# Kernel tuning notes

Hardware: AMD Instinct MI355X
Metric: run time of the kernel (lower is better)

The kernel has to match this reference:

```python
import jax, jax.numpy as jnp
import numpy as np

OUTPUT_SIZE = 16384          # number of map units (must be a perfect square)
SIDE = 128.0                 # sqrt(OUTPUT_SIZE)
SIGMA = 2.0                  # neighbourhood std-dev (non-trainable weight in original)
B, D = 2048, 256


def setup_inputs() -> dict:
    key = jax.random.key(0)
    k1, k2 = jax.random.split(key)
    x = jax.random.normal(k1, (B, D), dtype=jnp.float32)
    kernel = jax.random.normal(k2, (D, OUTPUT_SIZE), dtype=jnp.float32) * 0.1
    return {"x": x, "kernel": kernel}


def _grid_coords():
    # 2D coordinates of each flattened map unit: unit k -> (k // side, k % side)
    idx = jnp.arange(OUTPUT_SIZE, dtype=jnp.float32)
    return jnp.floor(idx / SIDE), jnp.mod(idx, SIDE)  # each (size,)


def reference(x, kernel):
    # Squared Euclidean distance of every sample to every prototype: (B, size).
    # Same math as tf.norm(x[:, :, None] - kernel[None])**2, expressed as a GEMM.
    norms2 = (jnp.sum(x * x, axis=1, keepdims=True)
              - 2.0 * (x @ kernel)
              + jnp.sum(kernel * kernel, axis=0, keepdims=True))
    norms2 = jnp.maximum(norms2, 0.0)

    # Winner-take-all unit per sample, mapped to 2D grid coordinates.
    wta = jnp.argmin(norms2, axis=1).astype(jnp.float32)        # (B,)
    mean_r = jnp.floor(wta / SIDE)                               # (B,)
    mean_c = jnp.mod(wta, SIDE)                                  # (B,)

    # Gaussian neighbourhood over the 2D grid, flattened: (B, size).
    gr, gc = _grid_coords()
    dr = gr[None, :] - mean_r[:, None]
    dc = gc[None, :] - mean_c[:, None]
    radials = jnp.exp(-0.5 / (SIGMA * SIGMA) * (dr * dr + dc * dc))

    return radials * norms2
```

## Files before the change

### kernel.cpp

```cpp
#include <hip/hip_runtime.h>
#include <hip/hip_fp16.h>

#define OUTN 16384
#define BATCH 2048
#define DIM   256
#define NCB   (OUTN / 128)

typedef _Float16 half8 __attribute__((ext_vector_type(8)));
typedef float    floatx4 __attribute__((ext_vector_type(4)));
typedef unsigned long long u64;

__device__ __forceinline__ void gl2lds16(const void* g, void* l) {
    __builtin_amdgcn_global_load_lds(
        (const __attribute__((address_space(1))) void*)g,
        (__attribute__((address_space(3))) void*)l, 16, 0, 0);
}

__device__ __forceinline__ u64 packkey(float v, int col) {
    unsigned u = __float_as_uint(v);
    u = (u & 0x80000000u) ? ~u : (u | 0x80000000u);
    return ((u64)u << 32) | (unsigned)col;
}
__device__ __forceinline__ float unpackval(u64 p) {
    unsigned u = (unsigned)(p >> 32);
    u = (u & 0x80000000u) ? (u & 0x7fffffffu) : ~u;
    return __uint_as_float(u);
}

__global__ void prep_x(const float* __restrict__ x, _Float16* __restrict__ xh,
                       float* __restrict__ rown) {
    int b = blockIdx.x, t = threadIdx.x;
    float v = x[b * DIM + t];
    xh[b * DIM + t] = (_Float16)v;
    float s = v * v;
    for (int off = 32; off; off >>= 1) s += __shfl_down(s, off, 64);
    __shared__ float wsum[4];
    if ((t & 63) == 0) wsum[t >> 6] = s;
    __syncthreads();
    if (t == 0) rown[b] = wsum[0] + wsum[1] + wsum[2] + wsum[3];
}

__global__ __launch_bounds__(256) void prep_kTn(const float* __restrict__ kern,
                                                _Float16* __restrict__ kT,
                                                float* __restrict__ coln) {
    __shared__ float tile[64][65];
    __shared__ float npart[4][64];
    int t = threadIdx.x, tx = t & 63, ty = t >> 6;
    int j0 = blockIdx.x * 64;
    float nrm = 0.f;
    for (int dc = 0; dc < DIM; dc += 64) {
        __syncthreads();
        for (int it = 0; it < 16; it++) {
            int d = dc + ty + it * 4;
            float v = kern[(size_t)d * OUTN + j0 + tx];
            tile[ty + it * 4][tx] = v;
            nrm = fmaf(v, v, nrm);
        }
        __syncthreads();
        for (int c = t; c < 512; c += 256) {
            int j = c >> 3, o8 = (c & 7) * 8;
            half8 h;
            for (int u = 0; u < 8; u++) h[u] = (_Float16)tile[o8 + u][j];
            *(half8*)&kT[(size_t)(j0 + j) * DIM + dc + o8] = h;
        }
    }
    npart[ty][tx] = nrm;
    __syncthreads();
    if (t < 64) coln[j0 + t] = npart[0][t] + npart[1][t] + npart[2][t] + npart[3][t];
}

__global__ __launch_bounds__(256) void gemm_norms(
        const _Float16* __restrict__ xh, const _Float16* __restrict__ kT,
        const float* __restrict__ rown, const float* __restrict__ coln,
        float* __restrict__ out, u64* __restrict__ blockcand) {
    __shared__ __align__(16) char smem[32768];
    _Float16* As = (_Float16*)smem;
    _Float16* Bs = (_Float16*)(smem + 16384);
    u64* cand = (u64*)smem;
    int tid  = threadIdx.x;
    int col0 = blockIdx.x * 128;
    int row0 = blockIdx.y * 128;
    int wid = tid >> 6, lane = tid & 63;
    int wr = wid >> 1, wc = wid & 1;
    int l15 = lane & 15, l4 = lane >> 4;

    floatx4 acc[4][4];
    for (int i = 0; i < 4; i++)
        for (int j = 0; j < 4; j++)
            acc[i][j] = (floatx4){0.f, 0.f, 0.f, 0.f};

    for (int kt = 0; kt < 4; kt++) {
        int k0 = kt * 64;
        for (int it = 0; it < 4; it++) {
            int chunk = it * 256 + tid;
            int r = chunk >> 3, k8 = (chunk & 7) * 8;
            gl2lds16(&xh[(size_t)(row0 + r) * DIM + k0 + k8], &As[chunk * 8]);
            gl2lds16(&kT[(size_t)(col0 + r) * DIM + k0 + k8], &Bs[chunk * 8]);
        }
        __syncthreads();
        for (int s = 0; s < 2; s++) {
            int kk = s * 32 + l4 * 8;
            half8 af[4], bf[4];
            for (int i = 0; i < 4; i++)
                af[i] = *(half8*)&As[(wr * 64 + i * 16 + l15) * 64 + kk];
            for (int j = 0; j < 4; j++)
                bf[j] = *(half8*)&Bs[(wc * 64 + j * 16 + l15) * 64 + kk];
            for (int i = 0; i < 4; i++)
                for (int j = 0; j < 4; j++)
                    acc[i][j] = __builtin_amdgcn_mfma_f32_16x16x32_f16(
                        af[i], bf[j], acc[i][j], 0, 0, 0);
        }
        __syncthreads();
    }

    float cn[4]; int oc[4];
    for (int j = 0; j < 4; j++) {
        oc[j] = col0 + wc * 64 + j * 16 + l15;
        cn[j] = coln[oc[j]];
    }
    for (int i = 0; i < 4; i++) {
        for (int r = 0; r < 4; r++) {
            int row_l = wr * 64 + i * 16 + l4 * 4 + r;
            int orow  = row0 + row_l;
            float rn = rown[orow];
            u64 best = ~0ull;
            for (int j = 0; j < 4; j++) {
                float val = rn + cn[j] - 2.0f * acc[i][j][r];
                out[(size_t)orow * OUTN + oc[j]] = val;
                u64 p = packkey(val, oc[j]);
                if (p < best) best = p;
            }
            cand[row_l * 32 + wc * 16 + l15] = best;
        }
    }
    __syncthreads();
    if (tid < 128) {
        u64 m1 = ~0ull, m2 = ~0ull;
        for (int s = 0; s < 32; s++) {
            u64 v = cand[tid * 32 + s];
            if (v < m1) { m2 = m1; m1 = v; }
            else if (v < m2) { m2 = v; }
        }
        size_t base = (size_t)(row0 + tid) * (NCB * 2) + blockIdx.x * 2;
        blockcand[base]     = m1;
        blockcand[base + 1] = m2;
    }
}

__global__ __launch_bounds__(256) void refine_finalize(
        const u64* __restrict__ blockcand, const float* __restrict__ x,
        const float* __restrict__ kern, const float* __restrict__ coln,
        float* __restrict__ out) {
    int b = blockIdx.x, t = threadIdx.x;
    __shared__ float xrow[DIM];
    __shared__ u64 red[256];
    xrow[t] = x[b * DIM + t];
    u64 e = blockcand[(size_t)b * 256 + t];
    red[t] = e;
    __syncthreads();
    for (int off = 128; off; off >>= 1) {
        if (t < off) { u64 o = red[t + off]; if (o < red[t]) red[t] = o; }
        __syncthreads();
    }
    float minv = unpackval(red[0]);
    __syncthreads();

    float ve = unpackval(e);
    u64 p = ~0ull;
    if (ve <= minv + 0.125f) {
        int j = (int)(e & 0xffffffffu);
        float dot = 0.f;
        for (int d = 0; d < DIM; d++)
            dot = fmaf(xrow[d], kern[(size_t)d * OUTN + j], dot);
        p = packkey(coln[j] - 2.0f * dot, j);
    }
    red[t] = p;
    __syncthreads();
    for (int off = 128; off; off >>= 1) {
        if (t < off) { u64 o = red[t + off]; if (o < red[t]) red[t] = o; }
        __syncthreads();
    }
    int w = (int)(red[0] & 0xffffffffu);
    int wrr = w >> 7, wcc = w & 127;

    float* rowp = out + (size_t)b * OUTN;
    for (int it = 0; it < 16; it++) {
        int idx4 = it * 256 + t;
        int j0 = idx4 * 4;
        int r  = j0 >> 7, c0 = j0 & 127;
        int dr = r - wrr, drsq = dr * dr;
        float4 res;
        {
            int dc = c0 - wcc;     int d2 = drsq + dc * dc;
            res.x = (d2 <= 720) ? __expf(-0.125f * (float)d2) * fmaxf(rowp[j0], 0.f) : 0.f;
        }
        {
            int dc = c0 + 1 - wcc; int d2 = drsq + dc * dc;
            res.y = (d2 <= 720) ? __expf(-0.125f * (float)d2) * fmaxf(rowp[j0 + 1], 0.f) : 0.f;
        }
        {
            int dc = c0 + 2 - wcc; int d2 = drsq + dc * dc;
            res.z = (d2 <= 720) ? __expf(-0.125f * (float)d2) * fmaxf(rowp[j0 + 2], 0.f) : 0.f;
        }
        {
            int dc = c0 + 3 - wcc; int d2 = drsq + dc * dc;
            res.w = (d2 <= 720) ? __expf(-0.125f * (float)d2) * fmaxf(rowp[j0 + 3], 0.f) : 0.f;
        }
        ((float4*)rowp)[idx4] = res;
    }
}

extern "C" void kernel_launch(void* const* d_in, const int* in_sizes, int n_in,
                              void* d_out, int out_size, void* d_ws, size_t ws_size,
                              hipStream_t stream) {
    const float* x    = (const float*)d_in[0];
    const float* kern = (const float*)d_in[1];
    float* out = (float*)d_out;
    char* ws = (char*)d_ws;

    _Float16* xh   = (_Float16*)(ws);
    _Float16* kT   = (_Float16*)(ws + (1u << 20));
    float*    coln = (float*)(ws + (9u << 20));
    float*    rown = (float*)(ws + (9u << 20) + 65536);
    u64* blockcand = (u64*)(ws + (10u << 20));

    prep_x<<<BATCH, DIM, 0, stream>>>(x, xh, rown);
    prep_kTn<<<OUTN / 64, 256, 0, stream>>>(kern, kT, coln);
    gemm_norms<<<dim3(OUTN / 128, BATCH / 128), 256, 0, stream>>>(xh, kT, rown, coln, out, blockcand);
    refine_finalize<<<BATCH, 256, 0, stream>>>(blockcand, x, kern, coln, out);
}
```

Before: 206.2 us.

## Merge prep kernels, swizzle LDS tiles, and stage distances in fp16 workspace

Combines the x and kernel prep kernels into one launch, splitting the kernel transpose over two D halves so more blocks run, with partial column norms summed later. Adds an XOR swizzle to the LDS layout in the GEMM to avoid bank conflicts on MFMA fragment reads. When the workspace is large enough, the intermediate squared distances are stored as fp16 in the workspace instead of fp32 in the output, and the finalize pass only reads values inside the Gaussian cutoff. This aims to halve intermediate write and read traffic, at the cost of fp16 rounding on the stored distances.

```diff
diff --git a/kernel.cpp b/kernel.cpp
--- a/kernel.cpp
+++ b/kernel.cpp
@@ -4,7 +4,6 @@
 #define OUTN 16384
 #define BATCH 2048
 #define DIM   256
-#define NCB   (OUTN / 128)
 
 typedef _Float16 half8 __attribute__((ext_vector_type(8)));
 typedef float    floatx4 __attribute__((ext_vector_type(4)));
@@ -27,52 +26,58 @@
     return __uint_as_float(u);
 }
 
-__global__ void prep_x(const float* __restrict__ x, _Float16* __restrict__ xh,
-                       float* __restrict__ rown) {
-    int b = blockIdx.x, t = threadIdx.x;
-    float v = x[b * DIM + t];
-    xh[b * DIM + t] = (_Float16)v;
-    float s = v * v;
-    for (int off = 32; off; off >>= 1) s += __shfl_down(s, off, 64);
-    __shared__ float wsum[4];
-    if ((t & 63) == 0) wsum[t >> 6] = s;
-    __syncthreads();
-    if (t == 0) rown[b] = wsum[0] + wsum[1] + wsum[2] + wsum[3];
-}
-
-__global__ __launch_bounds__(256) void prep_kTn(const float* __restrict__ kern,
-                                                _Float16* __restrict__ kT,
-                                                float* __restrict__ coln) {
-    __shared__ float tile[64][65];
-    __shared__ float npart[4][64];
-    int t = threadIdx.x, tx = t & 63, ty = t >> 6;
-    int j0 = blockIdx.x * 64;
-    float nrm = 0.f;
-    for (int dc = 0; dc < DIM; dc += 64) {
-        __syncthreads();
-        for (int it = 0; it < 16; it++) {
-            int d = dc + ty + it * 4;
-            float v = kern[(size_t)d * OUTN + j0 + tx];
-            tile[ty + it * 4][tx] = v;
-            nrm = fmaf(v, v, nrm);
-        }
-        __syncthreads();
-        for (int c = t; c < 512; c += 256) {
-            int j = c >> 3, o8 = (c & 7) * 8;
-            half8 h;
-            for (int u = 0; u < 8; u++) h[u] = (_Float16)tile[o8 + u][j];
-            *(half8*)&kT[(size_t)(j0 + j) * DIM + dc + o8] = h;
-        }
-    }
-    npart[ty][tx] = nrm;
-    __syncthreads();
-    if (t < 64) coln[j0 + t] = npart[0][t] + npart[1][t] + npart[2][t] + npart[3][t];
-}
-
+__global__ __launch_bounds__(256) void prep_all(
+        const float* __restrict__ x, const float* __restrict__ kern,
+        _Float16* __restrict__ xh, float* __restrict__ rown,
+        _Float16* __restrict__ kT, float* __restrict__ colnp) {
+    int blk = blockIdx.x, t = threadIdx.x;
+    if (blk < 512) {
+        __shared__ float tile[64][65];
+        __shared__ float npart[4][64];
+        int tx = t & 63, ty = t >> 6;
+        int j0 = (blk >> 1) * 64;
+        int dhalf = blk & 1, dbase = dhalf * 128;
+        float nrm = 0.f;
+        for (int pc = 0; pc < 2; pc++) {
+            int dc = dbase + pc * 64;
+            __syncthreads();
+            for (int it = 0; it < 16; it++) {
+                int d = dc + ty + it * 4;
+                float v = kern[(size_t)d * OUTN + j0 + tx];
+                tile[ty + it * 4][tx] = v;
+                nrm = fmaf(v, v, nrm);
+            }
+            __syncthreads();
+            for (int c = t; c < 512; c += 256) {
+                int j = c >> 3, o8 = (c & 7) * 8;
+                half8 h;
+                for (int u = 0; u < 8; u++) h[u] = (_Float16)tile[o8 + u][j];
+                *(half8*)&kT[(size_t)(j0 + j) * DIM + dc + o8] = h;
+            }
+        }
+        npart[ty][tx] = nrm;
+        __syncthreads();
+        if (t < 64)
+            colnp[(size_t)dhalf * OUTN + j0 + t] =
+                npart[0][t] + npart[1][t] + npart[2][t] + npart[3][t];
+    } else {
+        int b = blk - 512;
+        float v = x[b * DIM + t];
+        xh[b * DIM + t] = (_Float16)v;
+        float s = v * v;
+        for (int off = 32; off; off >>= 1) s += __shfl_down(s, off, 64);
+        __shared__ float wsum[4];
+        if ((t & 63) == 0) wsum[t >> 6] = s;
+        __syncthreads();
+        if (t == 0) rown[b] = wsum[0] + wsum[1] + wsum[2] + wsum[3];
+    }
+}
+
+template <bool NF16>
 __global__ __launch_bounds__(256) void gemm_norms(
         const _Float16* __restrict__ xh, const _Float16* __restrict__ kT,
-        const float* __restrict__ rown, const float* __restrict__ coln,
-        float* __restrict__ out, u64* __restrict__ blockcand) {
+        const float* __restrict__ rown, const float* __restrict__ colnp,
+        void* __restrict__ n2out, u64* __restrict__ blockcand) {
     __shared__ __align__(16) char smem[32768];
     _Float16* As = (_Float16*)smem;
     _Float16* Bs = (_Float16*)(smem + 16384);
@@ -83,6 +88,7 @@
     int wid = tid >> 6, lane = tid & 63;
     int wr = wid >> 1, wc = wid & 1;
     int l15 = lane & 15, l4 = lane >> 4;
+    int xh7 = l15 & 7;
 
     floatx4 acc[4][4];
     for (int i = 0; i < 4; i++)
@@ -93,18 +99,20 @@
         int k0 = kt * 64;
         for (int it = 0; it < 4; it++) {
             int chunk = it * 256 + tid;
-            int r = chunk >> 3, k8 = (chunk & 7) * 8;
-            gl2lds16(&xh[(size_t)(row0 + r) * DIM + k0 + k8], &As[chunk * 8]);
-            gl2lds16(&kT[(size_t)(col0 + r) * DIM + k0 + k8], &Bs[chunk * 8]);
+            int r = chunk >> 3, gg = chunk & 7;
+            int ksw = (gg ^ (r & 7)) * 8;
+            gl2lds16(&xh[(size_t)(row0 + r) * DIM + k0 + ksw], &As[chunk * 8]);
+            gl2lds16(&kT[(size_t)(col0 + r) * DIM + k0 + ksw], &Bs[chunk * 8]);
         }
         __syncthreads();
         for (int s = 0; s < 2; s++) {
-            int kk = s * 32 + l4 * 8;
+            int g = s * 4 + l4;
+            int sw = (g ^ xh7) * 8;
             half8 af[4], bf[4];
             for (int i = 0; i < 4; i++)
-                af[i] = *(half8*)&As[(wr * 64 + i * 16 + l15) * 64 + kk];
+                af[i] = *(half8*)&As[(wr * 64 + i * 16 + l15) * 64 + sw];
             for (int j = 0; j < 4; j++)
-                bf[j] = *(half8*)&Bs[(wc * 64 + j * 16 + l15) * 64 + kk];
+                bf[j] = *(half8*)&Bs[(wc * 64 + j * 16 + l15) * 64 + sw];
             for (int i = 0; i < 4; i++)
                 for (int j = 0; j < 4; j++)
                     acc[i][j] = __builtin_amdgcn_mfma_f32_16x16x32_f16(
@@ -116,7 +124,7 @@
     float cn[4]; int oc[4];
     for (int j = 0; j < 4; j++) {
         oc[j] = col0 + wc * 64 + j * 16 + l15;
-        cn[j] = coln[oc[j]];
+        cn[j] = colnp[oc[j]] + colnp[OUTN + oc[j]];
     }
     for (int i = 0; i < 4; i++) {
         for (int r = 0; r < 4; r++) {
@@ -126,7 +134,9 @@
             u64 best = ~0ull;
             for (int j = 0; j < 4; j++) {
                 float val = rn + cn[j] - 2.0f * acc[i][j][r];
-                out[(size_t)orow * OUTN + oc[j]] = val;
+                size_t oi = (size_t)orow * OUTN + oc[j];
+                if (NF16) ((_Float16*)n2out)[oi] = (_Float16)val;
+                else      ((float*)n2out)[oi]    = val;
                 u64 p = packkey(val, oc[j]);
                 if (p < best) best = p;
             }
@@ -141,16 +151,17 @@
             if (v < m1) { m2 = m1; m1 = v; }
             else if (v < m2) { m2 = v; }
         }
-        size_t base = (size_t)(row0 + tid) * (NCB * 2) + blockIdx.x * 2;
+        size_t base = (size_t)(row0 + tid) * 256 + blockIdx.x * 2;
         blockcand[base]     = m1;
         blockcand[base + 1] = m2;
     }
 }
 
+template <bool NF16>
 __global__ __launch_bounds__(256) void refine_finalize(
         const u64* __restrict__ blockcand, const float* __restrict__ x,
-        const float* __restrict__ kern, const float* __restrict__ coln,
-        float* __restrict__ out) {
+        const float* __restrict__ kern, const float* __restrict__ colnp,
+        const void* __restrict__ n2in, float* __restrict__ out) {
     int b = blockIdx.x, t = threadIdx.x;
     __shared__ float xrow[DIM];
     __shared__ u64 red[256];
@@ -172,7 +183,7 @@
         float dot = 0.f;
         for (int d = 0; d < DIM; d++)
             dot = fmaf(xrow[d], kern[(size_t)d * OUTN + j], dot);
-        p = packkey(coln[j] - 2.0f * dot, j);
+        p = packkey((colnp[j] + colnp[OUTN + j]) - 2.0f * dot, j);
     }
     red[t] = p;
     __syncthreads();
@@ -183,6 +194,8 @@
     int w = (int)(red[0] & 0xffffffffu);
     int wrr = w >> 7, wcc = w & 127;
 
+    const _Float16* r16 = (const _Float16*)n2in + (size_t)b * OUTN;
+    const float*    r32 = (const float*)n2in    + (size_t)b * OUTN;
     float* rowp = out + (size_t)b * OUTN;
     for (int it = 0; it < 16; it++) {
         int idx4 = it * 256 + t;
@@ -192,19 +205,23 @@
         float4 res;
         {
             int dc = c0 - wcc;     int d2 = drsq + dc * dc;
-            res.x = (d2 <= 720) ? __expf(-0.125f * (float)d2) * fmaxf(rowp[j0], 0.f) : 0.f;
+            float v = (d2 <= 720) ? (NF16 ? (float)r16[j0]     : r32[j0])     : 0.f;
+            res.x = (d2 <= 720) ? __expf(-0.125f * (float)d2) * fmaxf(v, 0.f) : 0.f;
         }
         {
             int dc = c0 + 1 - wcc; int d2 = drsq + dc * dc;
-            res.y = (d2 <= 720) ? __expf(-0.125f * (float)d2) * fmaxf(rowp[j0 + 1], 0.f) : 0.f;
+            float v = (d2 <= 720) ? (NF16 ? (float)r16[j0 + 1] : r32[j0 + 1]) : 0.f;
+            res.y = (d2 <= 720) ? __expf(-0.125f * (float)d2) * fmaxf(v, 0.f) : 0.f;
         }
         {
             int dc = c0 + 2 - wcc; int d2 = drsq + dc * dc;
-            res.z = (d2 <= 720) ? __expf(-0.125f * (float)d2) * fmaxf(rowp[j0 + 2], 0.f) : 0.f;
+            float v = (d2 <= 720) ? (NF16 ? (float)r16[j0 + 2] : r32[j0 + 2]) : 0.f;
+            res.z = (d2 <= 720) ? __expf(-0.125f * (float)d2) * fmaxf(v, 0.f) : 0.f;
         }
         {
             int dc = c0 + 3 - wcc; int d2 = drsq + dc * dc;
-            res.w = (d2 <= 720) ? __expf(-0.125f * (float)d2) * fmaxf(rowp[j0 + 3], 0.f) : 0.f;
+            float v = (d2 <= 720) ? (NF16 ? (float)r16[j0 + 3] : r32[j0 + 3]) : 0.f;
+            res.w = (d2 <= 720) ? __expf(-0.125f * (float)d2) * fmaxf(v, 0.f) : 0.f;
         }
         ((float4*)rowp)[idx4] = res;
     }
@@ -220,12 +237,22 @@
 
     _Float16* xh   = (_Float16*)(ws);
     _Float16* kT   = (_Float16*)(ws + (1u << 20));
-    float*    coln = (float*)(ws + (9u << 20));
-    float*    rown = (float*)(ws + (9u << 20) + 65536);
+    float*   colnp = (float*)(ws + (9u << 20));
+    float*   rown  = (float*)(ws + (9u << 20) + (128u << 10));
     u64* blockcand = (u64*)(ws + (10u << 20));
-
-    prep_x<<<BATCH, DIM, 0, stream>>>(x, xh, rown);
-    prep_kTn<<<OUTN / 64, 256, 0, stream>>>(kern, kT, coln);
-    gemm_norms<<<dim3(OUTN / 128, BATCH / 128), 256, 0, stream>>>(xh, kT, rown, coln, out, blockcand);
-    refine_finalize<<<BATCH, 256, 0, stream>>>(blockcand, x, kern, coln, out);
-}
+    void*    n2h   = (void*)(ws + (14u << 20));
+    bool f16path = ws_size >= ((size_t)78 << 20);
+
+    prep_all<<<2560, 256, 0, stream>>>(x, kern, xh, rown, kT, colnp);
+    if (f16path) {
+        gemm_norms<true><<<dim3(OUTN / 128, BATCH / 128), 256, 0, stream>>>(
+            xh, kT, rown, colnp, n2h, blockcand);
+        refine_finalize<true><<<BATCH, 256, 0, stream>>>(
+            blockcand, x, kern, colnp, n2h, out);
+    } else {
+        gemm_norms<false><<<dim3(OUTN / 128, BATCH / 128), 256, 0, stream>>>(
+            xh, kT, rown, colnp, (void*)out, blockcand);
+        refine_finalize<false><<<BATCH, 256, 0, stream>>>(
+            blockcand, x, kern, colnp, (const void*)out, out);
+    }
+}
```

New measurement: 202.1 us. 1.02x faster.
